# Kernel tuning notes

Hardware: AMD Instinct MI355X
Metric: run time of the kernel (lower is better)

Reference implementation:

```python
import jax, jax.numpy as jnp
import numpy as np

# ---- config (matches init_kwargs) ----
B = 4                 # batch_size
A = 262144            # anchors per example (1048576 total / 4)
PRE_NMS = 4000        # fpn_pre_nms_top_n
POST_NMS = 1000       # fpn_post_nms_top_n
NMS_THRESH = 0.3
AUG_THICK = 0.2       # nms_aug_thickness: minimum size used when computing IoU


def setup_inputs() -> dict:
    key = jax.random.key(0)
    k1, k2, k3, k4, k5 = jax.random.split(key, 5)
    N = B * A
    objectness = jax.random.normal(k1, (N,), dtype=jnp.float32)
    box_regression = 0.1 * jax.random.normal(k2, (N, 7), dtype=jnp.float32)
    # realistic anchors: centers in a 50m scene, sizes in [0.5, 4.0], yaw in [-pi, pi]
    centers = jax.random.uniform(k3, (N, 3), dtype=jnp.float32) * 50.0
    sizes = 0.5 + jax.random.uniform(k4, (N, 3), dtype=jnp.float32) * 3.5
    yaw = (jax.random.uniform(k5, (N, 1), dtype=jnp.float32) - 0.5) * (2.0 * np.pi)
    anchors = jnp.concatenate([centers, sizes, yaw], axis=-1)
    return {"objectness": objectness, "box_regression": box_regression, "anchors": anchors}


def _decode(reg, anc):
    # SECOND-style 3D box decode. anc/reg: [..., 7] = (x, y, z_bottom, sx, sy, sz, yaw)
    xa, ya, za, wa, la, ha, ra = [anc[..., i] for i in range(7)]
    dx, dy, dz, dw, dl, dh, dr = [reg[..., i] for i in range(7)]
    diag = jnp.sqrt(wa * wa + la * la)
    x = dx * diag + xa
    y = dy * diag + ya
    z = dz * ha + za
    w = jnp.exp(dw) * wa
    l = jnp.exp(dl) * la
    h = jnp.exp(dh) * ha
    r = dr + ra
    return jnp.stack([x, y, z, w, l, h, r], axis=-1)


def _iou3d_matrix(boxes, aug):
    # Axis-aligned 3D IoU with thickness augmentation (min size clamp).
    # boxes: [N, 7], 'yx_zb' mode -> z is the bottom of the box.
    x, y, z0 = boxes[:, 0], boxes[:, 1], boxes[:, 2]
    sx = jnp.maximum(boxes[:, 3], aug)
    sy = jnp.maximum(boxes[:, 4], aug)
    sz = jnp.maximum(boxes[:, 5], aug)
    lo = jnp.stack([x - sx / 2, y - sy / 2, z0], axis=-1)          # [N,3]
    hi = jnp.stack([x + sx / 2, y + sy / 2, z0 + sz], axis=-1)     # [N,3]
    inter_lo = jnp.maximum(lo[:, None, :], lo[None, :, :])         # [N,N,3]
    inter_hi = jnp.minimum(hi[:, None, :], hi[None, :, :])
    inter = jnp.prod(jnp.maximum(inter_hi - inter_lo, 0.0), axis=-1)  # [N,N]
    vol = sx * sy * sz
    union = vol[:, None] + vol[None, :] - inter
    return inter / jnp.maximum(union, 1e-8)


def _greedy_nms(iou, thresh):
    # boxes assumed sorted by descending score. Returns keep mask [N] (bool).
    n = iou.shape[0]
    idx = jnp.arange(n)

    def body(i, keep):
        cur = keep[i]
        suppress = (idx > i) & cur & (iou[i] > thresh)
        return keep & (~suppress)

    keep0 = jnp.ones((n,), dtype=bool)
    return jax.lax.fori_loop(0, n, body, keep0)


def _per_example(obj_logits, reg, anc):
    # obj_logits: [A], reg/anc: [A, 7]
    scores = jax.nn.sigmoid(obj_logits)
    top_scores, top_idx = jax.lax.top_k(scores, PRE_NMS)          # sorted desc
    boxes = _decode(reg[top_idx], anc[top_idx])                   # [PRE,7]
    iou = _iou3d_matrix(boxes, AUG_THICK)
    keep = _greedy_nms(iou, NMS_THRESH)
    # stable select: kept boxes first (score order preserved), take first POST_NMS
    rank_key = jnp.where(keep, 0, PRE_NMS) + jnp.arange(PRE_NMS)
    order = jnp.argsort(rank_key)
    sel = order[:POST_NMS]
    valid = keep[sel].astype(boxes.dtype)                         # [POST]
    out_boxes = boxes[sel] * valid[:, None]
    out_scores = top_scores[sel] * valid
    return jnp.concatenate([out_boxes, out_scores[:, None]], axis=-1)  # [POST,8]


def reference(objectness, box_regression, anchors):
    obj = objectness.reshape(B, A)
    reg = box_regression.reshape(B, A, 7)
    anc = anchors.reshape(B, A, 7)
    return jax.vmap(_per_example)(obj, reg, anc)                  # [B, POST, 8]
```

## Files before the change

kernel.cpp:

```cpp
#include <hip/hip_runtime.h>
#include <math.h>

typedef unsigned int u32;
typedef unsigned long long u64;

#define BB 4
#define AA 262144
#define NN (BB*AA)
#define PRE 4000
#define POST 1000
#define CAP 4096
#define CAPR 5632
#define MASKW 64
#define NBLK 63
#define NCHUNK 125
#define SLICES 64
#define RSLICE 8

static const size_t OFF_CNTG = 0;
static const size_t OFF_CNTE = 512;
static const size_t OFF_KEYS = 1024;
static const size_t OFF_RANK = OFF_KEYS + (size_t)BB*CAPR*8;
static const size_t ZERO_END = OFF_RANK + (size_t)BB*CAPR*4;
static const size_t OFF_HC   = ZERO_END;
static const size_t OFF_HF   = OFF_HC + 262144;
static const size_t OFF_P1   = OFF_HF + 262144;
static const size_t OFF_A1   = OFF_P1 + 128;
static const size_t OFF_P2   = OFF_A1 + 128;
static const size_t OFF_CROW = OFF_P2 + 128;
static const size_t OFF_NBOX = OFF_CROW + (size_t)BB*CAP*8*4;
static const size_t OFF_MASK = OFF_NBOX + (size_t)BB*CAP*8*4;

__device__ __forceinline__ u32 sigmoid_bits(float x) {
  float e = (float)exp(-(double)x);
  float s = 1.0f / (1.0f + e);
  return __float_as_uint(s);
}

__device__ __forceinline__ u32 mono_bits(float x) {
  u32 f = __float_as_uint(x);
  return (f & 0x80000000u) ? ~f : (f | 0x80000000u);
}

__global__ __launch_bounds__(256) void k_hcoarse(const float* __restrict__ obj,
                                                 u32* __restrict__ hc) {
  __shared__ u32 lh[256*16];
  int tid = threadIdx.x;
  for (int i = tid; i < 256*16; i += 256) lh[i] = 0;
  __syncthreads();
  size_t blockBase = (size_t)blockIdx.x * 4096;
  int rep = tid & 15;
  for (int k = 0; k < 16; ++k) {
    u32 tt = mono_bits(obj[blockBase + (size_t)k*256 + tid]);
    atomicAdd(&lh[(tt >> 24)*16 + rep], 1u);
  }
  __syncthreads();
  u32 s = 0;
  #pragma unroll
  for (int r = 0; r < 16; ++r) s += lh[tid*16 + r];
  hc[(size_t)blockIdx.x*256 + tid] = s;
}

__global__ __launch_bounds__(256) void k_res1(const u32* __restrict__ hc,
                                              u32* __restrict__ C_out,
                                              u32* __restrict__ acc_out) {
  int b = blockIdx.x, t = threadIdx.x;
  __shared__ u32 sum[256];
  const u32* base = hc + (size_t)b*SLICES*256;
  u32 s = 0;
  for (int k = 0; k < SLICES; ++k) s += base[k*256 + t];
  sum[t] = s;
  __syncthreads();
  if (t == 0) {
    u32 acc = 0; int cs = 0;
    for (int i = 255; i >= 0; --i) {
      u32 c = sum[i];
      if (acc + c >= (u32)PRE) { cs = i; break; }
      acc += c;
    }
    C_out[b] = (u32)cs; acc_out[b] = acc;
  }
}

__global__ __launch_bounds__(256) void k_hfine(const float* __restrict__ obj,
                                               const u32* __restrict__ C_in,
                                               u32* __restrict__ hf) {
  __shared__ u32 lh[256];
  int tid = threadIdx.x;
  lh[tid] = 0;
  __syncthreads();
  size_t blockBase = (size_t)blockIdx.x * 4096;
  int b = (int)(blockBase >> 18);
  u32 C = C_in[b];
  for (int k = 0; k < 16; ++k) {
    u32 tt = mono_bits(obj[blockBase + (size_t)k*256 + tid]);
    if ((tt >> 24) == C) atomicAdd(&lh[(tt >> 16) & 255u], 1u);
  }
  __syncthreads();
  hf[(size_t)blockIdx.x*256 + tid] = lh[tid];
}

__global__ __launch_bounds__(256) void k_res2(const u32* __restrict__ hf,
                                              const u32* __restrict__ C_in,
                                              const u32* __restrict__ acc_in,
                                              u32* __restrict__ P_out) {
  int b = blockIdx.x, t = threadIdx.x;
  __shared__ u32 sum[256];
  const u32* base = hf + (size_t)b*SLICES*256;
  u32 s = 0;
  for (int k = 0; k < SLICES; ++k) s += base[k*256 + t];
  sum[t] = s;
  __syncthreads();
  if (t == 0) {
    u32 acc = acc_in[b]; int fb = 0;
    for (int i = 255; i >= 0; --i) {
      u32 c = sum[i];
      if (acc + c >= (u32)PRE) { fb = i; break; }
      acc += c;
    }
    P_out[b] = (C_in[b] << 8) | (u32)fb;
  }
}

__global__ __launch_bounds__(256) void k_compact(const float* __restrict__ obj,
                                                 const u32* __restrict__ pfx,
                                                 int* __restrict__ cntG,
                                                 int* __restrict__ cntE,
                                                 u64* __restrict__ keys) {
  __shared__ u64 st[2048];
  __shared__ int nG, nE, baseG, baseE;
  int tid = threadIdx.x;
  if (tid == 0) { nG = 0; nE = 0; }
  __syncthreads();
  size_t blockBase = (size_t)blockIdx.x * 4096;
  int b = (int)(blockBase >> 18);
  u32 P = pfx[b];
  for (int k = 0; k < 16; ++k) {
    size_t g = blockBase + (size_t)k*256 + tid;
    float x = obj[g];
    u32 tb = mono_bits(x) >> 16;
    if (tb + 1u >= P) {
      u32 m = sigmoid_bits(x);
      u64 key = ((u64)m << 32) | (u64)(AA - 1 - (u32)(g & (AA - 1)));
      if (tb > P) { int p = atomicAdd(&nG, 1); if (p < 1536) st[p] = key; }
      else        { int p = atomicAdd(&nE, 1); if (p < 512) st[2047 - p] = key; }
    }
  }
  __syncthreads();
  int ng = nG < 1536 ? nG : 1536;
  int ne = nE < 512 ? nE : 512;
  if (tid == 0) baseG = atomicAdd(&cntG[b*32], ng);
  if (tid == 1) baseE = atomicAdd(&cntE[b*32], ne);
  __syncthreads();
  for (int i = tid; i < ng; i += 256) {
    int p = baseG + i;
    if (p < 4000) keys[(size_t)b*CAPR + p] = st[i];
  }
  for (int i = tid; i < ne; i += 256) {
    int p = baseE + i;
    if (p < CAPR - 4000) keys[(size_t)b*CAPR + 4000 + p] = st[2047 - i];
  }
}

__global__ __launch_bounds__(64) void k_rankp(const u64* __restrict__ keys,
                                              u32* __restrict__ rank) {
  int b = blockIdx.z;
  int slot = blockIdx.x*64 + threadIdx.x;
  const u64* kb = keys + (size_t)b*CAPR;
  u64 myk = kb[slot];
  const ulonglong2* p2 = (const ulonglong2*)(kb + blockIdx.y*(CAPR/RSLICE));
  int r = 0;
  for (int base = 0; base < CAPR/(2*RSLICE); base += 16) {
    ulonglong2 v[16];
    #pragma unroll
    for (int k = 0; k < 16; ++k) v[k] = p2[base + k];
    #pragma unroll
    for (int k = 0; k < 16; ++k)
      r += (int)(v[k].x > myk) + (int)(v[k].y > myk);
  }
  if (r) atomicAdd(&rank[b*CAPR + slot], (u32)r);
}

__global__ __launch_bounds__(256) void k_decode(const u64* __restrict__ keys,
                                                const u32* __restrict__ rank,
                                                const float* __restrict__ reg,
                                                const float* __restrict__ anc,
                                                float* __restrict__ crow,
                                                float* __restrict__ nbox) {
  int t = blockIdx.x*256 + threadIdx.x;
  int b = t / CAPR, slot = t - b*CAPR;
  u64 myk = keys[(size_t)b*CAPR + slot];
  int rk = (int)rank[b*CAPR + slot];
  if (myk == 0 || rk >= PRE) return;
  u32 m = (u32)(myk >> 32);
  int idx = AA - 1 - (int)(myk & 0xFFFFFFFFull);
  float score = __uint_as_float(m);
  size_t g = ((size_t)b << 18) + (size_t)idx;
  const float* rg = reg + g*7;
  const float* an = anc + g*7;
  float xa=an[0], ya=an[1], za=an[2], wa=an[3], la=an[4], ha=an[5], ra=an[6];
  float dx=rg[0], dy=rg[1], dz=rg[2], dw=rg[3], dl=rg[4], dh=rg[5], dr=rg[6];
  float diag = sqrtf(wa*wa + la*la);
  float x = dx*diag + xa;
  float y = dy*diag + ya;
  float z = dz*ha + za;
  float w = expf(dw)*wa;
  float l = expf(dl)*la;
  float h = expf(dh)*ha;
  float r = dr + ra;
  float* cr = crow + ((size_t)b*CAP + rk)*8;
  cr[0]=x; cr[1]=y; cr[2]=z; cr[3]=w; cr[4]=l; cr[5]=h; cr[6]=r; cr[7]=score;
  float sx = fmaxf(w, 0.2f), sy = fmaxf(l, 0.2f), sz = fmaxf(h, 0.2f);
  float* nb = nbox + ((size_t)b*CAP + rk)*8;
  nb[0]=x - sx*0.5f; nb[1]=y - sy*0.5f; nb[2]=z;
  nb[3]=x + sx*0.5f; nb[4]=y + sy*0.5f; nb[5]=z + sz;
  nb[6]=sx*sy*sz;   nb[7]=0.f;
}

__global__ __launch_bounds__(256) void k_mask(const float* __restrict__ nbox,
                                              u64* __restrict__ mask) {
  int c = blockIdx.x;
  int R = blockIdx.y;
  int b = blockIdx.z;
  if (c < R*4) return;
  __shared__ float4 ca4[64], cb4[64];
  int t = threadIdx.x;
  int j0 = c*64;
  if (t < 64) {
    int j = j0 + t; int jc = j < PRE ? j : 0;
    const float4* p = (const float4*)(nbox + ((size_t)b*CAP + jc)*8);
    ca4[t] = p[0]; cb4[t] = p[1];
  }
  __syncthreads();
  int i = R*256 + t;
  if (i >= PRE) return;
  const float4* rp = (const float4*)(nbox + ((size_t)b*CAP + i)*8);
  float4 A = rp[0], Bv = rp[1];
  u64 bits = 0;
  #pragma unroll
  for (int jj = 0; jj < 64; ++jj) {
    float4 C = ca4[jj], D = cb4[jj];
    float d0 = fminf(A.w,  C.w) - fmaxf(A.x, C.x);
    float d1 = fminf(Bv.x, D.x) - fmaxf(A.y, C.y);
    float d2 = fminf(Bv.y, D.y) - fmaxf(A.z, C.z);
    float inter = fmaxf(d0, 0.f) * fmaxf(d1, 0.f) * fmaxf(d2, 0.f);
    float uni = Bv.z + D.z - inter;
    if (inter > 0.3f * uni) bits |= (1ull << jj);
  }
  int vcols = PRE - j0;
  if (vcols < 64) bits &= ((1ull << vcols) - 1ull);
  if (j0 <= i) {
    int d = i - j0;
    if (d >= 63) bits = 0;
    else bits &= ~((2ull << d) - 1ull);
  }
  mask[((size_t)b*MASKW + c)*PRE + i] = bits;
}

__device__ __forceinline__ void load_chunk(u64 (&buf)[32], const u64* col,
                                           int c, int lane) {
  bool act = lane >= (c >> 1);
  const ulonglong2* p = (const ulonglong2*)(col + c*32);
  #pragma unroll
  for (int k = 0; k < 16; ++k) {
    ulonglong2 v; v.x = 0; v.y = 0;
    if (act) v = p[k];
    buf[2*k] = v.x; buf[2*k+1] = v.y;
  }
}

__device__ __forceinline__ void resolve_chunk(u64 (&buf)[32], int c, int lane,
                                              u64& removed, int& kc,
                                              int* __restrict__ sel_lds) {
  int wq = c >> 1;
  int base = (c & 1) * 32;
  u64 cur = removed, km = 0;
  #pragma unroll
  for (int jj = 0; jj < 32; ++jj) {
    if (((cur >> (base + jj)) & 1ull) == 0ull) {
      km |= (1ull << (base + jj));
      cur |= buf[jj];
    }
  }
  u64 kmw = __shfl(km, wq, 64);
  #pragma unroll
  for (int jj = 0; jj < 32; ++jj) {
    if ((kmw >> (base + jj)) & 1ull) removed |= buf[jj];
  }
  int sh = base + (lane & 31);
  bool mine = (lane < 32) && ((kmw >> sh) & 1ull);
  int pos = kc + (int)__popcll(kmw & ((1ull << sh) - 1ull));
  if (mine && pos < POST) sel_lds[pos] = c*32 + lane;
  kc += (int)__popcll(kmw);
}

__global__ __launch_bounds__(64) void k_reduce(const u64* __restrict__ mask,
                                               const float* __restrict__ crow,
                                               float* __restrict__ out) {
  __shared__ int sel_lds[POST];
  int b = blockIdx.x, lane = threadIdx.x;
  const u64* col = mask + ((size_t)b*MASKW + lane)*PRE;
  u64 bufA[32], bufB[32];
  u64 removed = 0;
  int kc = 0;
  load_chunk(bufA, col, 0, lane);
  for (int c = 0; c < NCHUNK; c += 2) {
    if (c + 1 < NCHUNK) load_chunk(bufB, col, c + 1, lane);
    resolve_chunk(bufA, c, lane, removed, kc, sel_lds);
    if (kc >= POST) break;
    if (c + 1 >= NCHUNK) break;
    if (c + 2 < NCHUNK) load_chunk(bufA, col, c + 2, lane);
    resolve_chunk(bufB, c + 1, lane, removed, kc, sel_lds);
    if (kc >= POST) break;
  }
  __syncthreads();
  int kcap = kc < POST ? kc : POST;
  for (int r = lane; r < POST; r += 64) {
    float4 o0 = make_float4(0.f,0.f,0.f,0.f), o1 = o0;
    if (r < kcap) {
      int i = sel_lds[r];
      const float4* p = (const float4*)(crow + ((size_t)b*CAP + i)*8);
      o0 = p[0]; o1 = p[1];
    }
    float4* q = (float4*)(out + ((size_t)b*POST + r)*8);
    q[0] = o0; q[1] = o1;
  }
}

extern "C" void kernel_launch(void* const* d_in, const int* in_sizes, int n_in,
                              void* d_out, int out_size, void* d_ws, size_t ws_size,
                              hipStream_t stream) {
  const float* obj = (const float*)d_in[0];
  const float* reg = (const float*)d_in[1];
  const float* anc = (const float*)d_in[2];
  float* out = (float*)d_out;
  char* ws = (char*)d_ws;

  int*  cntG = (int*)(ws + OFF_CNTG);
  int*  cntE = (int*)(ws + OFF_CNTE);
  u64*  keys = (u64*)(ws + OFF_KEYS);
  u32*  rank = (u32*)(ws + OFF_RANK);
  u32*  hc   = (u32*)(ws + OFF_HC);
  u32*  hf   = (u32*)(ws + OFF_HF);
  u32*  P1   = (u32*)(ws + OFF_P1);
  u32*  A1   = (u32*)(ws + OFF_A1);
  u32*  P2   = (u32*)(ws + OFF_P2);
  float* crow = (float*)(ws + OFF_CROW);
  float* nbox = (float*)(ws + OFF_NBOX);
  u64*  mask = (u64*)(ws + OFF_MASK);

  (void)hipMemsetAsync(ws, 0, ZERO_END, stream);

  k_hcoarse<<<NN/4096, 256, 0, stream>>>(obj, hc);
  k_res1<<<BB, 256, 0, stream>>>(hc, P1, A1);
  k_hfine<<<NN/4096, 256, 0, stream>>>(obj, P1, hf);
  k_res2<<<BB, 256, 0, stream>>>(hf, P1, A1, P2);
  k_compact<<<NN/4096, 256, 0, stream>>>(obj, P2, cntG, cntE, keys);
  k_rankp<<<dim3(CAPR/64, RSLICE, BB), 64, 0, stream>>>(keys, rank);
  k_decode<<<(BB*CAPR)/256, 256, 0, stream>>>(keys, rank, reg, anc, crow, nbox);
  k_mask<<<dim3(NBLK, 16, BB), 256, 0, stream>>>(nbox, mask);
  k_reduce<<<BB, 64, 0, stream>>>(mask, crow, out);
}
```

Before: 222.1 us.

## Stream NMS mask chunks through a 4-deep async global-to-LDS pipeline

The serial NMS reduce kernel now prefetches mask chunks with global_load_lds 16-byte async copies into a 4-slot LDS ring buffer, replacing the double-buffered register loads. Hand-placed vmcnt and lgkmcnt waits keep up to three chunks in flight while the current chunk is resolved. The aim is to hide global-memory latency in this latency-bound single-wave loop. It drops the per-lane load predicate, so every lane now loads, and it relies on exact waitcnt counting and about 64KB of LDS staging.

```diff
diff --git a/kernel.cpp b/kernel.cpp
--- a/kernel.cpp
+++ b/kernel.cpp
@@ -16,6 +16,7 @@
 #define NCHUNK 125
 #define SLICES 64
 #define RSLICE 8
+#define RDEPTH 4
 
 static const size_t OFF_CNTG = 0;
 static const size_t OFF_CNTE = 512;
@@ -30,6 +31,11 @@
 static const size_t OFF_CROW = OFF_P2 + 128;
 static const size_t OFF_NBOX = OFF_CROW + (size_t)BB*CAP*8*4;
 static const size_t OFF_MASK = OFF_NBOX + (size_t)BB*CAP*8*4;
+
+#define ASYNC_CP16(gsrc, ldst) \
+  __builtin_amdgcn_global_load_lds( \
+      (__attribute__((address_space(1))) const void*)(gsrc), \
+      (__attribute__((address_space(3))) void*)(ldst), 16, 0, 0)
 
 __device__ __forceinline__ u32 sigmoid_bits(float x) {
   float e = (float)exp(-(double)x);
@@ -257,18 +263,6 @@
   mask[((size_t)b*MASKW + c)*PRE + i] = bits;
 }
 
-__device__ __forceinline__ void load_chunk(u64 (&buf)[32], const u64* col,
-                                           int c, int lane) {
-  bool act = lane >= (c >> 1);
-  const ulonglong2* p = (const ulonglong2*)(col + c*32);
-  #pragma unroll
-  for (int k = 0; k < 16; ++k) {
-    ulonglong2 v; v.x = 0; v.y = 0;
-    if (act) v = p[k];
-    buf[2*k] = v.x; buf[2*k+1] = v.y;
-  }
-}
-
 __device__ __forceinline__ void resolve_chunk(u64 (&buf)[32], int c, int lane,
                                               u64& removed, int& kc,
                                               int* __restrict__ sel_lds) {
@@ -297,20 +291,43 @@
 __global__ __launch_bounds__(64) void k_reduce(const u64* __restrict__ mask,
                                                const float* __restrict__ crow,
                                                float* __restrict__ out) {
+  __shared__ __align__(16) u64 stage[RDEPTH*2048];
   __shared__ int sel_lds[POST];
   int b = blockIdx.x, lane = threadIdx.x;
   const u64* col = mask + ((size_t)b*MASKW + lane)*PRE;
-  u64 bufA[32], bufB[32];
+
+  #pragma unroll
+  for (int p = 0; p < RDEPTH-1; ++p) {
+    const u64* src = col + p*32;
+    #pragma unroll
+    for (int k = 0; k < 16; ++k)
+      ASYNC_CP16(src + 2*k, (char*)stage + p*16384 + k*1024);
+  }
+
   u64 removed = 0;
   int kc = 0;
-  load_chunk(bufA, col, 0, lane);
-  for (int c = 0; c < NCHUNK; c += 2) {
-    if (c + 1 < NCHUNK) load_chunk(bufB, col, c + 1, lane);
-    resolve_chunk(bufA, c, lane, removed, kc, sel_lds);
-    if (kc >= POST) break;
-    if (c + 1 >= NCHUNK) break;
-    if (c + 2 < NCHUNK) load_chunk(bufA, col, c + 2, lane);
-    resolve_chunk(bufB, c + 1, lane, removed, kc, sel_lds);
+  for (int c = 0; c < NCHUNK; ++c) {
+    if (c <= NCHUNK-3)      asm volatile("s_waitcnt vmcnt(32)" ::: "memory");
+    else if (c == NCHUNK-2) asm volatile("s_waitcnt vmcnt(16)" ::: "memory");
+    else                    asm volatile("s_waitcnt vmcnt(0)"  ::: "memory");
+    __builtin_amdgcn_sched_barrier(0);
+    if (c + RDEPTH - 1 < NCHUNK) {
+      asm volatile("s_waitcnt lgkmcnt(0)" ::: "memory");
+      int slot = (c + RDEPTH - 1) & (RDEPTH - 1);
+      const u64* src = col + (c + RDEPTH - 1)*32;
+      #pragma unroll
+      for (int k = 0; k < 16; ++k)
+        ASYNC_CP16(src + 2*k, (char*)stage + slot*16384 + k*1024);
+    }
+    u64 buf[32];
+    const ulonglong2* sp =
+        (const ulonglong2*)((const char*)stage + (c & (RDEPTH-1))*16384 + lane*16);
+    #pragma unroll
+    for (int k = 0; k < 16; ++k) {
+      ulonglong2 v = sp[(size_t)k*64];
+      buf[2*k] = v.x; buf[2*k+1] = v.y;
+    }
+    resolve_chunk(buf, c, lane, removed, kc, sel_lds);
     if (kc >= POST) break;
   }
   __syncthreads();
```

After: 260.6 us. +17.3%, slower.

## Distribute NMS reduce chunks across 8 waves with LDS token-passing

Applied to the files above, without the earlier changes.

The serial greedy-NMS reduce kernel now runs 8 waves per block. Each wave prefetches its own chunks of the suppression mask into registers ahead of time. The waves take turns resolving chunks in order, passing the removed-bitmask and kept count through LDS and an atomic flag. This hides global-memory load latency that a single wave could not cover with two buffers. The cost is spin-wait synchronisation between waves and prefetch loads that are wasted after early termination.

```diff
diff --git a/kernel.cpp b/kernel.cpp
--- a/kernel.cpp
+++ b/kernel.cpp
@@ -16,6 +16,8 @@
 #define NCHUNK 125
 #define SLICES 64
 #define RSLICE 8
+#define RWAVES 8
+#define STOPVAL 0x7fffffff
 
 static const size_t OFF_CNTG = 0;
 static const size_t OFF_CNTE = 512;
@@ -294,28 +296,65 @@
   kc += (int)__popcll(kmw);
 }
 
-__global__ __launch_bounds__(64) void k_reduce(const u64* __restrict__ mask,
-                                               const float* __restrict__ crow,
-                                               float* __restrict__ out) {
+__global__ __launch_bounds__(RWAVES*64, 2) void k_reduce(const u64* __restrict__ mask,
+                                                         const float* __restrict__ crow,
+                                                         float* __restrict__ out) {
+  __shared__ u64 rem_lds[64];
   __shared__ int sel_lds[POST];
-  int b = blockIdx.x, lane = threadIdx.x;
+  __shared__ int kc_lds;
+  __shared__ int flag;
+  int b = blockIdx.x;
+  int tid = threadIdx.x;
+  int w = tid >> 6;
+  int lane = tid & 63;
   const u64* col = mask + ((size_t)b*MASKW + lane)*PRE;
+  if (tid < 64) rem_lds[tid] = 0;
+  if (tid == 0) { kc_lds = 0; flag = 0; }
+  __syncthreads();
+
   u64 bufA[32], bufB[32];
-  u64 removed = 0;
-  int kc = 0;
-  load_chunk(bufA, col, 0, lane);
-  for (int c = 0; c < NCHUNK; c += 2) {
-    if (c + 1 < NCHUNK) load_chunk(bufB, col, c + 1, lane);
-    resolve_chunk(bufA, c, lane, removed, kc, sel_lds);
-    if (kc >= POST) break;
-    if (c + 1 >= NCHUNK) break;
-    if (c + 2 < NCHUNK) load_chunk(bufA, col, c + 2, lane);
-    resolve_chunk(bufB, c + 1, lane, removed, kc, sel_lds);
-    if (kc >= POST) break;
-  }
-  __syncthreads();
+  load_chunk(bufA, col, w, lane);
+  load_chunk(bufB, col, w + RWAVES, lane);
+
+  auto turn = [&](u64 (&buf)[32], int c) -> bool {
+    int v;
+    for (;;) {
+      v = __hip_atomic_load(&flag, __ATOMIC_ACQUIRE, __HIP_MEMORY_SCOPE_WORKGROUP);
+      if (v >= c) break;
+      __builtin_amdgcn_s_sleep(1);
+    }
+    if (v != c) return true;
+    __builtin_amdgcn_s_waitcnt(0);
+    u64 removed = rem_lds[lane];
+    int kc = kc_lds;
+    resolve_chunk(buf, c, lane, removed, kc, sel_lds);
+    rem_lds[lane] = removed;
+    if (lane == 0) kc_lds = kc;
+    __threadfence_block();
+    int nf = (kc >= POST || c + 1 >= NCHUNK) ? STOPVAL : c + 1;
+    __hip_atomic_store(&flag, nf, __ATOMIC_RELEASE, __HIP_MEMORY_SCOPE_WORKGROUP);
+    return nf == STOPVAL;
+  };
+
+  bool stop = false;
+  int c = w;
+  while (!stop) {
+    stop = turn(bufA, c);
+    if (!stop && c + 2*RWAVES < NCHUNK)
+      load_chunk(bufA, col, c + 2*RWAVES, lane);
+    c += RWAVES;
+    if (stop || c >= NCHUNK) break;
+    stop = turn(bufB, c);
+    if (!stop && c + 2*RWAVES < NCHUNK)
+      load_chunk(bufB, col, c + 2*RWAVES, lane);
+    c += RWAVES;
+    if (c >= NCHUNK) break;
+  }
+
+  __syncthreads();
+  int kc = kc_lds;
   int kcap = kc < POST ? kc : POST;
-  for (int r = lane; r < POST; r += 64) {
+  for (int r = tid; r < POST; r += RWAVES*64) {
     float4 o0 = make_float4(0.f,0.f,0.f,0.f), o1 = o0;
     if (r < kcap) {
       int i = sel_lds[r];
@@ -359,5 +398,5 @@
   k_rankp<<<dim3(CAPR/64, RSLICE, BB), 64, 0, stream>>>(keys, rank);
   k_decode<<<(BB*CAPR)/256, 256, 0, stream>>>(keys, rank, reg, anc, crow, nbox);
   k_mask<<<dim3(NBLK, 16, BB), 256, 0, stream>>>(nbox, mask);
-  k_reduce<<<BB, 64, 0, stream>>>(mask, crow, out);
-}
+  k_reduce<<<BB, RWAVES*64, 0, stream>>>(mask, crow, out);
+}
```

New measurement: 228.9 us. 3.0% more time.

## Fold histogram resolve kernels and workspace memset into neighbouring kernels

Applied to the files above, without the earlier changes.

Removes the two tiny per-batch resolve kernels (k_res1, k_res2) and the hipMemsetAsync by having every block of k_hfine and k_compact redundantly sum the histogram slices and scan for the threshold bucket itself. k_hcoarse now zeroes the counter/key/rank workspace. This cuts three launches and their serialization gaps from the critical path. In exchange, each of the 256 blocks re-reads 64 KB of histogram data and runs a serial 256-step scan on one thread.

```diff
diff --git a/kernel.cpp b/kernel.cpp
--- a/kernel.cpp
+++ b/kernel.cpp
@@ -24,10 +24,7 @@
 static const size_t ZERO_END = OFF_RANK + (size_t)BB*CAPR*4;
 static const size_t OFF_HC   = ZERO_END;
 static const size_t OFF_HF   = OFF_HC + 262144;
-static const size_t OFF_P1   = OFF_HF + 262144;
-static const size_t OFF_A1   = OFF_P1 + 128;
-static const size_t OFF_P2   = OFF_A1 + 128;
-static const size_t OFF_CROW = OFF_P2 + 128;
+static const size_t OFF_CROW = OFF_HF + 262144 + 384;
 static const size_t OFF_NBOX = OFF_CROW + (size_t)BB*CAP*8*4;
 static const size_t OFF_MASK = OFF_NBOX + (size_t)BB*CAP*8*4;
 
@@ -43,10 +40,13 @@
 }
 
 __global__ __launch_bounds__(256) void k_hcoarse(const float* __restrict__ obj,
-                                                 u32* __restrict__ hc) {
+                                                 u32* __restrict__ hc,
+                                                 u64* __restrict__ zws) {
   __shared__ u32 lh[256*16];
   int tid = threadIdx.x;
   for (int i = tid; i < 256*16; i += 256) lh[i] = 0;
+  int zidx = blockIdx.x*256 + tid;
+  if (zidx < (int)(ZERO_END/8)) zws[zidx] = 0;
   __syncthreads();
   size_t blockBase = (size_t)blockIdx.x * 4096;
   int rep = tid & 15;
@@ -61,37 +61,34 @@
   hc[(size_t)blockIdx.x*256 + tid] = s;
 }
 
-__global__ __launch_bounds__(256) void k_res1(const u32* __restrict__ hc,
-                                              u32* __restrict__ C_out,
-                                              u32* __restrict__ acc_out) {
-  int b = blockIdx.x, t = threadIdx.x;
+__global__ __launch_bounds__(256) void k_hfine(const float* __restrict__ obj,
+                                               const u32* __restrict__ hc,
+                                               u32* __restrict__ hf) {
   __shared__ u32 sum[256];
-  const u32* base = hc + (size_t)b*SLICES*256;
-  u32 s = 0;
-  for (int k = 0; k < SLICES; ++k) s += base[k*256 + t];
-  sum[t] = s;
-  __syncthreads();
-  if (t == 0) {
+  __shared__ u32 lh[256];
+  __shared__ u32 Cs;
+  int tid = threadIdx.x;
+  size_t blockBase = (size_t)blockIdx.x * 4096;
+  int b = (int)(blockBase >> 18);
+  {
+    const u32* basep = hc + (size_t)b*SLICES*256;
+    u32 s = 0;
+    for (int k = 0; k < SLICES; ++k) s += basep[k*256 + tid];
+    sum[tid] = s;
+  }
+  lh[tid] = 0;
+  __syncthreads();
+  if (tid == 0) {
     u32 acc = 0; int cs = 0;
     for (int i = 255; i >= 0; --i) {
       u32 c = sum[i];
       if (acc + c >= (u32)PRE) { cs = i; break; }
       acc += c;
     }
-    C_out[b] = (u32)cs; acc_out[b] = acc;
-  }
-}
-
-__global__ __launch_bounds__(256) void k_hfine(const float* __restrict__ obj,
-                                               const u32* __restrict__ C_in,
-                                               u32* __restrict__ hf) {
-  __shared__ u32 lh[256];
-  int tid = threadIdx.x;
-  lh[tid] = 0;
-  __syncthreads();
-  size_t blockBase = (size_t)blockIdx.x * 4096;
-  int b = (int)(blockBase >> 18);
-  u32 C = C_in[b];
+    Cs = (u32)cs;
+  }
+  __syncthreads();
+  u32 C = Cs;
   for (int k = 0; k < 16; ++k) {
     u32 tt = mono_bits(obj[blockBase + (size_t)k*256 + tid]);
     if ((tt >> 24) == C) atomicAdd(&lh[(tt >> 16) & 255u], 1u);
@@ -100,41 +97,55 @@
   hf[(size_t)blockIdx.x*256 + tid] = lh[tid];
 }
 
-__global__ __launch_bounds__(256) void k_res2(const u32* __restrict__ hf,
-                                              const u32* __restrict__ C_in,
-                                              const u32* __restrict__ acc_in,
-                                              u32* __restrict__ P_out) {
-  int b = blockIdx.x, t = threadIdx.x;
+__global__ __launch_bounds__(256) void k_compact(const float* __restrict__ obj,
+                                                 const u32* __restrict__ hc,
+                                                 const u32* __restrict__ hf,
+                                                 int* __restrict__ cntG,
+                                                 int* __restrict__ cntE,
+                                                 u64* __restrict__ keys) {
   __shared__ u32 sum[256];
-  const u32* base = hf + (size_t)b*SLICES*256;
-  u32 s = 0;
-  for (int k = 0; k < SLICES; ++k) s += base[k*256 + t];
-  sum[t] = s;
-  __syncthreads();
-  if (t == 0) {
-    u32 acc = acc_in[b]; int fb = 0;
+  __shared__ u64 st[2048];
+  __shared__ int nG, nE, baseG, baseE;
+  __shared__ u32 Cs, As, Ps;
+  int tid = threadIdx.x;
+  size_t blockBase = (size_t)blockIdx.x * 4096;
+  int b = (int)(blockBase >> 18);
+  {
+    const u32* basep = hc + (size_t)b*SLICES*256;
+    u32 s = 0;
+    for (int k = 0; k < SLICES; ++k) s += basep[k*256 + tid];
+    sum[tid] = s;
+  }
+  if (tid == 0) { nG = 0; nE = 0; }
+  __syncthreads();
+  if (tid == 0) {
+    u32 acc = 0; int cs = 0;
+    for (int i = 255; i >= 0; --i) {
+      u32 c = sum[i];
+      if (acc + c >= (u32)PRE) { cs = i; break; }
+      acc += c;
+    }
+    Cs = (u32)cs; As = acc;
+  }
+  __syncthreads();
+  {
+    const u32* basep = hf + (size_t)b*SLICES*256;
+    u32 s = 0;
+    for (int k = 0; k < SLICES; ++k) s += basep[k*256 + tid];
+    sum[tid] = s;
+  }
+  __syncthreads();
+  if (tid == 0) {
+    u32 acc = As; int fb = 0;
     for (int i = 255; i >= 0; --i) {
       u32 c = sum[i];
       if (acc + c >= (u32)PRE) { fb = i; break; }
       acc += c;
     }
-    P_out[b] = (C_in[b] << 8) | (u32)fb;
-  }
-}
-
-__global__ __launch_bounds__(256) void k_compact(const float* __restrict__ obj,
-                                                 const u32* __restrict__ pfx,
-                                                 int* __restrict__ cntG,
-                                                 int* __restrict__ cntE,
-                                                 u64* __restrict__ keys) {
-  __shared__ u64 st[2048];
-  __shared__ int nG, nE, baseG, baseE;
-  int tid = threadIdx.x;
-  if (tid == 0) { nG = 0; nE = 0; }
-  __syncthreads();
-  size_t blockBase = (size_t)blockIdx.x * 4096;
-  int b = (int)(blockBase >> 18);
-  u32 P = pfx[b];
+    Ps = (Cs << 8) | (u32)fb;
+  }
+  __syncthreads();
+  u32 P = Ps;
   for (int k = 0; k < 16; ++k) {
     size_t g = blockBase + (size_t)k*256 + tid;
     float x = obj[g];
@@ -342,20 +353,13 @@
   u32*  rank = (u32*)(ws + OFF_RANK);
   u32*  hc   = (u32*)(ws + OFF_HC);
   u32*  hf   = (u32*)(ws + OFF_HF);
-  u32*  P1   = (u32*)(ws + OFF_P1);
-  u32*  A1   = (u32*)(ws + OFF_A1);
-  u32*  P2   = (u32*)(ws + OFF_P2);
   float* crow = (float*)(ws + OFF_CROW);
   float* nbox = (float*)(ws + OFF_NBOX);
   u64*  mask = (u64*)(ws + OFF_MASK);
 
-  (void)hipMemsetAsync(ws, 0, ZERO_END, stream);
-
-  k_hcoarse<<<NN/4096, 256, 0, stream>>>(obj, hc);
-  k_res1<<<BB, 256, 0, stream>>>(hc, P1, A1);
-  k_hfine<<<NN/4096, 256, 0, stream>>>(obj, P1, hf);
-  k_res2<<<BB, 256, 0, stream>>>(hf, P1, A1, P2);
-  k_compact<<<NN/4096, 256, 0, stream>>>(obj, P2, cntG, cntE, keys);
+  k_hcoarse<<<NN/4096, 256, 0, stream>>>(obj, hc, (u64*)ws);
+  k_hfine<<<NN/4096, 256, 0, stream>>>(obj, hc, hf);
+  k_compact<<<NN/4096, 256, 0, stream>>>(obj, hc, hf, cntG, cntE, keys);
   k_rankp<<<dim3(CAPR/64, RSLICE, BB), 64, 0, stream>>>(keys, rank);
   k_decode<<<(BB*CAPR)/256, 256, 0, stream>>>(keys, rank, reg, anc, crow, nbox);
   k_mask<<<dim3(NBLK, 16, BB), 256, 0, stream>>>(nbox, mask);
```

Result: no change. 218.0 us (-1.8%).
